# Optimization experiments

Measured on AMD Instinct MI355X. Metric: run time of the kernel, lower is better.

## Reference

```python
import jax, jax.numpy as jnp
import numpy as np

B, S, I, H = 64, 512, 512, 1024


def setup_inputs() -> dict:
    key = jax.random.key(0)
    ks = jax.random.split(key, 5)
    bound = 1.0 / np.sqrt(H)  # nn.GRUCell default init
    u = lambda k, shape: jax.random.uniform(k, shape, jnp.float32, -bound, bound)
    return {
        "input": jax.random.normal(ks[0], (B, S, I), jnp.float32),
        "state": jnp.zeros((B, H), jnp.float32),
        "weight_ih": u(ks[1], (3 * H, I)),
        "weight_hh": u(ks[2], (3 * H, H)),
        "bias_ih": u(ks[3], (3 * H,)),
        "bias_hh": u(ks[4], (3 * H,)),
        "gamma_ih": jnp.ones((3 * H,), jnp.float32),
        "gamma_hh": jnp.ones((3 * H,), jnp.float32),
    }


def _ln_x(x, g, b):
    # kefirski's _layer_norm_x: (x - mean) / std (unbiased std, eps=0)
    mean = jnp.mean(x, axis=-1, keepdims=True)
    std = jnp.std(x, axis=-1, keepdims=True, ddof=1)
    return g * ((x - mean) / std) + b


def _ln_h(x, g, b):
    # kefirski's _layer_norm_h: mean-subtraction only
    return g * (x - jnp.mean(x, axis=-1, keepdims=True)) + b


def reference(input, state, weight_ih, weight_hh, bias_ih, bias_hh, gamma_ih, gamma_hh):
    Hd = state.shape[-1]
    # Input-side projections + LN are h-independent -> precompute over all timesteps
    ih = jnp.einsum("bsi,gi->bsg", input, weight_ih)  # [B,S,3H]
    ih_rz = _ln_x(ih[..., : 2 * Hd], gamma_ih[: 2 * Hd], bias_ih[: 2 * Hd])  # [B,S,2H]
    ih_n = _ln_x(ih[..., 2 * Hd :], gamma_ih[2 * Hd :], bias_ih[2 * Hd :])  # [B,S,H]

    def step(h, xs):
        irz, inn = xs  # [B,2H], [B,H]
        hh = h @ weight_hh.T  # [B,3H]
        hh_rz = _ln_h(hh[:, : 2 * Hd], gamma_hh[: 2 * Hd], bias_hh[: 2 * Hd])
        hh_n = _ln_h(hh[:, 2 * Hd :], gamma_hh[2 * Hd :], bias_hh[2 * Hd :])
        rz = jax.nn.sigmoid(irz + hh_rz)
        r, z = rz[:, :Hd], rz[:, Hd:]
        n = jnp.tanh(inn + r * hh_n)
        h_new = (1.0 - z) * n + z * h
        return h_new, h_new

    final_state, outs = jax.lax.scan(
        step, state, (ih_rz.transpose(1, 0, 2), ih_n.transpose(1, 0, 2))
    )
    return outs.transpose(1, 0, 2), final_state  # [B,S,H], [B,H]
```

## Files before the change

kernel.cpp:

```cpp
#include <hip/hip_runtime.h>
#include <stdint.h>
#include <stddef.h>

#define B_  64
#define S_  512
#define I_  512
#define H_  1024
#define G_  3072
#define NWG 64
#define CPW 32

typedef short short8 __attribute__((ext_vector_type(8)));
typedef float f32x4  __attribute__((ext_vector_type(4)));
typedef unsigned short u16x4 __attribute__((ext_vector_type(4)));

__device__ __forceinline__ unsigned short f32_to_bf16(float f){
  unsigned u = __builtin_bit_cast(unsigned, f);
  u = (u + 0x7FFFu + ((u >> 16) & 1u)) >> 16;
  return (unsigned short)u;
}
__device__ __forceinline__ float bf16_to_f32(unsigned short s){
  unsigned u = ((unsigned)s) << 16;
  return __builtin_bit_cast(float, u);
}
__device__ __forceinline__ float sig_(float x){ return 1.0f/(1.0f + __expf(-x)); }
__device__ __forceinline__ float tanh_(float x){
  float ax = fabsf(x);
  float t = __expf(-2.0f*ax);
  float r = (1.0f - t)/(1.0f + t);
  return copysignf(r, x);
}

__device__ __forceinline__ short8 ldg16_coh(const unsigned short* p){
  short8 r;
  asm volatile("global_load_dwordx4 %0, %1, off sc0 sc1" : "=v"(r) : "v"(p) : "memory");
  return r;
}
__device__ __forceinline__ void stg8_coh(unsigned short* p, u16x4 v){
  asm volatile("global_store_dwordx2 %0, %1, off sc0 sc1" :: "v"(p), "v"(v) : "memory");
}
__device__ __forceinline__ void stg4_coh(unsigned* p, unsigned v){
  asm volatile("global_store_dword %0, %1, off sc0 sc1" :: "v"(p), "v"(v) : "memory");
}
__device__ __forceinline__ unsigned ldg4_coh_wait(const unsigned* p){
  unsigned r;
  asm volatile("global_load_dword %0, %1, off sc0 sc1\n\ts_waitcnt vmcnt(0)"
               : "=v"(r) : "v"(p) : "memory");
  return r;
}
__device__ __forceinline__ u16x4 ldg8(const unsigned short* p){
  u16x4 r;
  asm volatile("global_load_dwordx2 %0, %1, off" : "=v"(r) : "v"(p) : "memory");
  return r;
}

__global__ __launch_bounds__(256) void k_cvt4(const float* __restrict__ src,
                                              unsigned short* __restrict__ dst, int n4){
  int i = blockIdx.x*blockDim.x + threadIdx.x;
  int st = gridDim.x*blockDim.x;
  for (; i < n4; i += st){
    f32x4 v = *(const f32x4*)(src + (size_t)i*4);
    u16x4 o;
    o[0]=f32_to_bf16(v[0]); o[1]=f32_to_bf16(v[1]);
    o[2]=f32_to_bf16(v[2]); o[3]=f32_to_bf16(v[3]);
    *(u16x4*)(dst + (size_t)i*4) = o;
  }
}

__global__ __launch_bounds__(256) void k_cmean(const float* __restrict__ whh,
                                               unsigned short* __restrict__ CM){
  int k = blockIdx.x*256 + threadIdx.x;
  float s0 = 0.f, s1 = 0.f;
  for (int j = 0; j < 2048; ++j) s0 += whh[(size_t)j*H_ + k];
  for (int j = 2048; j < 3072; ++j) s1 += whh[(size_t)j*H_ + k];
  CM[k]      = f32_to_bf16(s0 * (1.0f/2048.0f));
  CM[H_ + k] = f32_to_bf16(s1 * (1.0f/1024.0f));
  for (int r = 2; r < 16; ++r) CM[(size_t)r*H_ + k] = 0;
}

__global__ __launch_bounds__(256, 2) void k_gemm_ih(
    const unsigned short* __restrict__ X,
    const unsigned short* __restrict__ W,
    unsigned short* __restrict__ IH)
{
  __shared__ __align__(16) short As[128*32];
  __shared__ __align__(16) short Bs[128*32];
  int bid = blockIdx.x;
  int mt = bid / 24, nt = bid % 24;
  int tid = threadIdx.x, lane = tid & 63, wid = tid >> 6;
  int vr = wid >> 1, vc = wid & 1;
  int r0s = tid >> 2, r1s = r0s + 64;
  int sc = (tid & 3) * 8;
  const unsigned short* xa0 = X + (size_t)(mt*128 + r0s)*512 + sc;
  const unsigned short* xa1 = X + (size_t)(mt*128 + r1s)*512 + sc;
  const unsigned short* wb0 = W + (size_t)(nt*128 + r0s)*512 + sc;
  const unsigned short* wb1 = W + (size_t)(nt*128 + r1s)*512 + sc;

  f32x4 acc[4][4];
  #pragma unroll
  for (int m=0;m<4;m++)
    #pragma unroll
    for (int n=0;n<4;n++) acc[m][n] = (f32x4){0.f,0.f,0.f,0.f};

  short8 ra0 = *(const short8*)xa0;
  short8 ra1 = *(const short8*)xa1;
  short8 rb0 = *(const short8*)wb0;
  short8 rb1 = *(const short8*)wb1;
  int ko = (lane >> 4) * 8;

  for (int kt = 0; kt < 16; ++kt){
    __syncthreads();
    *(short8*)&As[r0s*32 + sc] = ra0;
    *(short8*)&As[r1s*32 + sc] = ra1;
    *(short8*)&Bs[r0s*32 + sc] = rb0;
    *(short8*)&Bs[r1s*32 + sc] = rb1;
    __syncthreads();
    if (kt < 15){
      ra0 = *(const short8*)(xa0 + (kt+1)*32);
      ra1 = *(const short8*)(xa1 + (kt+1)*32);
      rb0 = *(const short8*)(wb0 + (kt+1)*32);
      rb1 = *(const short8*)(wb1 + (kt+1)*32);
    }
    short8 af[4], bfr[4];
    #pragma unroll
    for (int m=0;m<4;m++) af[m]  = *(const short8*)&As[(vr*64 + m*16 + (lane&15))*32 + ko];
    #pragma unroll
    for (int n=0;n<4;n++) bfr[n] = *(const short8*)&Bs[(vc*64 + n*16 + (lane&15))*32 + ko];
    #pragma unroll
    for (int m=0;m<4;m++)
      #pragma unroll
      for (int n=0;n<4;n++)
        acc[m][n] = __builtin_amdgcn_mfma_f32_16x16x32_bf16(af[m], bfr[n], acc[m][n], 0,0,0);
  }
  int row0 = mt*128 + vr*64, col0 = nt*128 + vc*64;
  int rl = (lane >> 4) * 4, cl = lane & 15;
  #pragma unroll
  for (int m=0;m<4;m++)
    #pragma unroll
    for (int n=0;n<4;n++)
      #pragma unroll
      for (int r=0;r<4;r++){
        int row = row0 + m*16 + rl + r;
        int rowT = ((row & 511) << 6) | (row >> 9);
        IH[(size_t)rowT*G_ + (col0 + n*16 + cl)] = f32_to_bf16(acc[m][n][r]);
      }
}

__global__ __launch_bounds__(256) void k_ln(
    unsigned short* __restrict__ IH,
    const float* __restrict__ gih,
    const float* __restrict__ bih)
{
  __shared__ float red[4][4];
  int row = blockIdx.x, tid = threadIdx.x, lane = tid & 63, wid = tid >> 6;
  unsigned short* p = IH + (size_t)row * G_;
  float xv[3][4];
  #pragma unroll
  for (int q=0;q<3;q++){
    u16x4 v = *(const u16x4*)(p + (tid + q*256)*4);
    #pragma unroll
    for (int j=0;j<4;j++) xv[q][j] = bf16_to_f32(v[j]);
  }
  float s0=0, q0=0, s1=0, q1=0;
  #pragma unroll
  for (int q=0;q<2;q++)
    #pragma unroll
    for (int j=0;j<4;j++){ s0 += xv[q][j]; q0 += xv[q][j]*xv[q][j]; }
  #pragma unroll
  for (int j=0;j<4;j++){ s1 += xv[2][j]; q1 += xv[2][j]*xv[2][j]; }
  #pragma unroll
  for (int off=32; off>0; off>>=1){
    s0 += __shfl_down(s0, off, 64);
    q0 += __shfl_down(q0, off, 64);
    s1 += __shfl_down(s1, off, 64);
    q1 += __shfl_down(q1, off, 64);
  }
  if (lane == 0){ red[wid][0]=s0; red[wid][1]=q0; red[wid][2]=s1; red[wid][3]=q1; }
  __syncthreads();
  float S0 = red[0][0]+red[1][0]+red[2][0]+red[3][0];
  float Q0 = red[0][1]+red[1][1]+red[2][1]+red[3][1];
  float S1 = red[0][2]+red[1][2]+red[2][2]+red[3][2];
  float Q1 = red[0][3]+red[1][3]+red[2][3]+red[3][3];
  float m0 = S0 * (1.0f/2048.0f);
  float rs0 = rsqrtf(fmaxf((Q0 - S0*m0) * (1.0f/2047.0f), 1e-20f));
  float m1 = S1 * (1.0f/1024.0f);
  float rs1 = rsqrtf(fmaxf((Q1 - S1*m1) * (1.0f/1023.0f), 1e-20f));
  #pragma unroll
  for (int q=0;q<3;q++){
    int base = (tid + q*256)*4;
    u16x4 o;
    #pragma unroll
    for (int j=0;j<4;j++){
      int col = base + j;
      float y = (q<2) ? (xv[q][j]-m0)*rs0 : (xv[q][j]-m1)*rs1;
      o[j] = f32_to_bf16(gih[col]*y + bih[col]);
    }
    *(u16x4*)(p + base) = o;
  }
}

__global__ __launch_bounds__(256, 1) void k_gru(
    const unsigned short* __restrict__ IH,
    const unsigned short* __restrict__ WHH,
    const unsigned short* __restrict__ CM,
    unsigned short* __restrict__ HB,
    const float* __restrict__ ghh,
    const float* __restrict__ bhh,
    const float* __restrict__ state,
    float* __restrict__ out,
    unsigned* __restrict__ FLAGS)
{
  __shared__ float PSUM[4][112][34];
  const int g = blockIdx.x & 31;
  const int p = blockIdx.x >> 5;
  const int tid = threadIdx.x;
  const int lane = tid & 63;
  const int wv = tid >> 6;
  const int l15 = lane & 15;
  const int lho = (lane >> 4) << 3;
  const int colbase = g * CPW;
  const int rowbase = p * 32;

  short8 bfr[7][8];
  #pragma unroll
  for (int ct = 0; ct < 7; ++ct){
    const unsigned short* src = (ct < 6)
        ? (WHH + (size_t)((ct>>1)*H_ + colbase + (ct&1)*16 + l15)*H_)
        : (CM + (size_t)l15*H_);
    #pragma unroll
    for (int ks = 0; ks < 8; ++ks)
      bfr[ct][ks] = *(const short8*)(src + wv*256 + ks*32 + lho);
  }

  const int b_ = tid & 31;
  const int cq = tid >> 5;
  const int c0 = colbase + cq*4;
  const int gb = rowbase + b_;
  float gr[4],gz[4],gn[4],br_[4],bz_[4],bn_[4],hv[4];
  #pragma unroll
  for (int j = 0; j < 4; ++j){
    gr[j] = ghh[c0+j];   gz[j] = ghh[H_+c0+j];   gn[j] = ghh[2*H_+c0+j];
    br_[j]= bhh[c0+j];   bz_[j]= bhh[H_+c0+j];   bn_[j]= bhh[2*H_+c0+j];
    hv[j] = state[(size_t)gb*H_ + c0 + j];
  }

  const unsigned* myflag = FLAGS + (p*32 + (lane & 31))*16;
  int cur = 0;

  for (int t = 0; t < S_; ++t){
    const unsigned short* ihp = IH + ((size_t)t*B_ + gb)*G_;
    u16x4 ir  = ldg8(ihp + c0);
    u16x4 izv = ldg8(ihp + H_ + c0);
    u16x4 inv = ldg8(ihp + 2*H_ + c0);

    for (;;){
      unsigned v = ldg4_coh_wait(myflag);
      if (__all((int)(v >= (unsigned)t))) break;
    }

    const unsigned short* hb = HB + cur*(B_*H_);
    short8 af[8][2];
    #pragma unroll
    for (int ks = 0; ks < 8; ++ks)
      #pragma unroll
      for (int rt = 0; rt < 2; ++rt)
        af[ks][rt] = ldg16_coh(hb + (size_t)(rowbase + rt*16 + l15)*H_ + wv*256 + ks*32 + lho);

    f32x4 acc[7][2];
    #pragma unroll
    for (int ct = 0; ct < 7; ++ct)
      #pragma unroll
      for (int rt = 0; rt < 2; ++rt)
        acc[ct][rt] = (f32x4){0.f,0.f,0.f,0.f};

    #pragma unroll
    for (int ks = 0; ks < 8; ++ks){
      asm volatile("s_waitcnt vmcnt(%0)" :: "i"(14 - 2*ks) : "memory");
      __builtin_amdgcn_sched_barrier(0);
      #pragma unroll
      for (int rt = 0; rt < 2; ++rt)
        #pragma unroll
        for (int ct = 0; ct < 7; ++ct)
          acc[ct][rt] = __builtin_amdgcn_mfma_f32_16x16x32_bf16(af[ks][rt], bfr[ct][ks], acc[ct][rt], 0,0,0);
    }

    #pragma unroll
    for (int ct = 0; ct < 7; ++ct)
      #pragma unroll
      for (int rt = 0; rt < 2; ++rt)
        *(f32x4*)&PSUM[wv][ct*16 + l15][rt*16 + (lane>>4)*4] = acc[ct][rt];
    __syncthreads();

    float hhr[4]={0,0,0,0}, hhz[4]={0,0,0,0}, hhn[4]={0,0,0,0};
    float mrz = 0.f, mn = 0.f;
    #pragma unroll
    for (int w = 0; w < 4; ++w){
      #pragma unroll
      for (int j = 0; j < 4; ++j){
        hhr[j] += PSUM[w][cq*4 + j][b_];
        hhz[j] += PSUM[w][32 + cq*4 + j][b_];
        hhn[j] += PSUM[w][64 + cq*4 + j][b_];
      }
      mrz += PSUM[w][96][b_];
      mn  += PSUM[w][97][b_];
    }
    f32x4 ho;
    #pragma unroll
    for (int j = 0; j < 4; ++j){
      float R = sig_(bf16_to_f32(ir[j])  + gr[j]*(hhr[j]-mrz) + br_[j]);
      float Z = sig_(bf16_to_f32(izv[j]) + gz[j]*(hhz[j]-mrz) + bz_[j]);
      float N = tanh_(bf16_to_f32(inv[j]) + R*(gn[j]*(hhn[j]-mn) + bn_[j]));
      hv[j] = (1.0f - Z)*N + Z*hv[j];
      ho[j] = hv[j];
    }
    u16x4 h16;
    #pragma unroll
    for (int j = 0; j < 4; ++j) h16[j] = f32_to_bf16(hv[j]);
    stg8_coh(HB + (cur^1)*(B_*H_) + (size_t)gb*H_ + c0, h16);

    asm volatile("s_waitcnt vmcnt(0)" ::: "memory");
    __syncthreads();
    if (tid == 0) stg4_coh((unsigned*)(FLAGS + (p*32 + g)*16), (unsigned)(t+1));
    *(f32x4*)(out + ((size_t)gb*S_ + t)*H_ + c0) = ho;
    cur ^= 1;
  }
  #pragma unroll
  for (int j = 0; j < 4; ++j)
    out[(size_t)B_*S_*H_ + (size_t)gb*H_ + c0 + j] = hv[j];
}

extern "C" void kernel_launch(void* const* d_in, const int* in_sizes, int n_in,
                              void* d_out, int out_size, void* d_ws, size_t ws_size,
                              hipStream_t stream){
  (void)in_sizes; (void)n_in; (void)out_size; (void)ws_size;
  const float* x   = (const float*)d_in[0];
  const float* st  = (const float*)d_in[1];
  const float* wih = (const float*)d_in[2];
  const float* whh = (const float*)d_in[3];
  const float* bih = (const float*)d_in[4];
  const float* bhh = (const float*)d_in[5];
  const float* gih = (const float*)d_in[6];
  const float* ghh = (const float*)d_in[7];
  float* out = (float*)d_out;
  char* ws = (char*)d_ws;

  unsigned short* IH    = (unsigned short*)(ws);
  unsigned short* X16   = (unsigned short*)(ws + 201326592ull);
  unsigned short* WIH16 = (unsigned short*)(ws + 234881024ull);
  unsigned short* WHH16 = (unsigned short*)(ws + 238026752ull);
  unsigned short* CM16  = (unsigned short*)(ws + 244318208ull);
  unsigned short* HB    = (unsigned short*)(ws + 244350976ull);
  unsigned*       FLAGS = (unsigned*)      (ws + 244613120ull);

  hipMemsetAsync(FLAGS, 0, 4096, stream);
  k_cvt4<<<2048, 256, 0, stream>>>(x,   X16,   4194304);
  k_cvt4<<<1024, 256, 0, stream>>>(wih, WIH16, 393216);
  k_cvt4<<<1024, 256, 0, stream>>>(whh, WHH16, 786432);
  k_cvt4<<<64,   256, 0, stream>>>(st,  HB,    16384);
  k_cmean<<<4,   256, 0, stream>>>(whh, CM16);
  k_gemm_ih<<<6144, 256, 0, stream>>>(X16, WIH16, IH);
  k_ln<<<32768, 256, 0, stream>>>(IH, gih, bih);
  k_gru<<<NWG, 256, 0, stream>>>(IH, WHH16, CM16, HB, ghh, bhh, st, out, FLAGS);
}
```

Measured before the change: 3.052 ms.

## Fuse input LayerNorm stats into GEMM epilogue and stream h loads per flag

Removes the separate LayerNorm kernel. The IH GEMM epilogue now accumulates per-row sum and sum-of-squares into a STAT buffer with atomics, and the recurrent kernel applies the normalization on the fly when it loads IH. The flag wait is also reworked: each lane polls a specific producer's flag and issues its h-state loads for a k-slice as soon as that producer is ready, instead of waiting for all producers first. This saves a full read/write pass over the large IH buffer and may overlap synchronization with loads. In exchange it adds float atomics, extra per-step normalization arithmetic, and stats computed from fp32 accumulators rather than the bf16-rounded values.

```diff
diff --git a/kernel.cpp b/kernel.cpp
--- a/kernel.cpp
+++ b/kernel.cpp
@@ -42,10 +42,9 @@
 __device__ __forceinline__ void stg4_coh(unsigned* p, unsigned v){
   asm volatile("global_store_dword %0, %1, off sc0 sc1" :: "v"(p), "v"(v) : "memory");
 }
-__device__ __forceinline__ unsigned ldg4_coh_wait(const unsigned* p){
+__device__ __forceinline__ unsigned ldg4_coh(const unsigned* p){
   unsigned r;
-  asm volatile("global_load_dword %0, %1, off sc0 sc1\n\ts_waitcnt vmcnt(0)"
-               : "=v"(r) : "v"(p) : "memory");
+  asm volatile("global_load_dword %0, %1, off sc0 sc1" : "=v"(r) : "v"(p) : "memory");
   return r;
 }
 __device__ __forceinline__ u16x4 ldg8(const unsigned short* p){
@@ -81,7 +80,8 @@
 __global__ __launch_bounds__(256, 2) void k_gemm_ih(
     const unsigned short* __restrict__ X,
     const unsigned short* __restrict__ W,
-    unsigned short* __restrict__ IH)
+    unsigned short* __restrict__ IH,
+    float* __restrict__ STAT)
 {
   __shared__ __align__(16) short As[128*32];
   __shared__ __align__(16) short Bs[128*32];
@@ -144,59 +144,27 @@
         int rowT = ((row & 511) << 6) | (row >> 9);
         IH[(size_t)rowT*G_ + (col0 + n*16 + cl)] = f32_to_bf16(acc[m][n][r]);
       }
-}
-
-__global__ __launch_bounds__(256) void k_ln(
-    unsigned short* __restrict__ IH,
-    const float* __restrict__ gih,
-    const float* __restrict__ bih)
-{
-  __shared__ float red[4][4];
-  int row = blockIdx.x, tid = threadIdx.x, lane = tid & 63, wid = tid >> 6;
-  unsigned short* p = IH + (size_t)row * G_;
-  float xv[3][4];
-  #pragma unroll
-  for (int q=0;q<3;q++){
-    u16x4 v = *(const u16x4*)(p + (tid + q*256)*4);
-    #pragma unroll
-    for (int j=0;j<4;j++) xv[q][j] = bf16_to_f32(v[j]);
-  }
-  float s0=0, q0=0, s1=0, q1=0;
-  #pragma unroll
-  for (int q=0;q<2;q++)
-    #pragma unroll
-    for (int j=0;j<4;j++){ s0 += xv[q][j]; q0 += xv[q][j]*xv[q][j]; }
-  #pragma unroll
-  for (int j=0;j<4;j++){ s1 += xv[2][j]; q1 += xv[2][j]*xv[2][j]; }
-  #pragma unroll
-  for (int off=32; off>0; off>>=1){
-    s0 += __shfl_down(s0, off, 64);
-    q0 += __shfl_down(q0, off, 64);
-    s1 += __shfl_down(s1, off, 64);
-    q1 += __shfl_down(q1, off, 64);
-  }
-  if (lane == 0){ red[wid][0]=s0; red[wid][1]=q0; red[wid][2]=s1; red[wid][3]=q1; }
-  __syncthreads();
-  float S0 = red[0][0]+red[1][0]+red[2][0]+red[3][0];
-  float Q0 = red[0][1]+red[1][1]+red[2][1]+red[3][1];
-  float S1 = red[0][2]+red[1][2]+red[2][2]+red[3][2];
-  float Q1 = red[0][3]+red[1][3]+red[2][3]+red[3][3];
-  float m0 = S0 * (1.0f/2048.0f);
-  float rs0 = rsqrtf(fmaxf((Q0 - S0*m0) * (1.0f/2047.0f), 1e-20f));
-  float m1 = S1 * (1.0f/1024.0f);
-  float rs1 = rsqrtf(fmaxf((Q1 - S1*m1) * (1.0f/1023.0f), 1e-20f));
-  #pragma unroll
-  for (int q=0;q<3;q++){
-    int base = (tid + q*256)*4;
-    u16x4 o;
-    #pragma unroll
-    for (int j=0;j<4;j++){
-      int col = base + j;
-      float y = (q<2) ? (xv[q][j]-m0)*rs0 : (xv[q][j]-m1)*rs1;
-      o[j] = f32_to_bf16(gih[col]*y + bih[col]);
+
+  const int soff = (nt < 16) ? 0 : 2;
+  #pragma unroll
+  for (int m=0;m<4;m++)
+    #pragma unroll
+    for (int r=0;r<4;r++){
+      float s1 = 0.f, s2 = 0.f;
+      #pragma unroll
+      for (int n=0;n<4;n++){ float v = acc[m][n][r]; s1 += v; s2 += v*v; }
+      #pragma unroll
+      for (int off=1; off<16; off<<=1){
+        s1 += __shfl_xor(s1, off, 16);
+        s2 += __shfl_xor(s2, off, 16);
+      }
+      if (cl == 0){
+        int row = row0 + m*16 + rl + r;
+        float* sp = STAT + (size_t)row*4 + soff;
+        atomicAdd(sp,     s1);
+        atomicAdd(sp + 1, s2);
+      }
     }
-    *(u16x4*)(p + base) = o;
-  }
 }
 
 __global__ __launch_bounds__(256, 1) void k_gru(
@@ -206,6 +174,9 @@
     unsigned short* __restrict__ HB,
     const float* __restrict__ ghh,
     const float* __restrict__ bhh,
+    const float* __restrict__ gih,
+    const float* __restrict__ bih,
+    const float* __restrict__ STAT,
     const float* __restrict__ state,
     float* __restrict__ out,
     unsigned* __restrict__ FLAGS)
@@ -236,35 +207,50 @@
   const int cq = tid >> 5;
   const int c0 = colbase + cq*4;
   const int gb = rowbase + b_;
-  float gr[4],gz[4],gn[4],br_[4],bz_[4],bn_[4],hv[4];
+  float gr[4],gz[4],gn[4],br_[4],bz_[4],bn_[4];
+  float gir[4],giz[4],gin[4],bir[4],biz[4],bin[4],hv[4];
   #pragma unroll
   for (int j = 0; j < 4; ++j){
-    gr[j] = ghh[c0+j];   gz[j] = ghh[H_+c0+j];   gn[j] = ghh[2*H_+c0+j];
-    br_[j]= bhh[c0+j];   bz_[j]= bhh[H_+c0+j];   bn_[j]= bhh[2*H_+c0+j];
-    hv[j] = state[(size_t)gb*H_ + c0 + j];
-  }
-
-  const unsigned* myflag = FLAGS + (p*32 + (lane & 31))*16;
-  int cur = 0;
+    int col = c0 + j;
+    gr[j] = ghh[col];   gz[j] = ghh[H_+col];   gn[j] = ghh[2*H_+col];
+    br_[j]= bhh[col];   bz_[j]= bhh[H_+col];   bn_[j]= bhh[2*H_+col];
+    gir[j]= gih[col];   giz[j]= gih[H_+col];   gin[j]= gih[2*H_+col];
+    bir[j]= bih[col];   biz[j]= bih[H_+col];   bin[j]= bih[2*H_+col];
+    hv[j] = state[(size_t)gb*H_ + col];
+  }
+
+  const unsigned* fbase = FLAGS + (size_t)(p*32 + wv*8 + (lane & 7))*16;
+  unsigned* pubflag = FLAGS + (size_t)(p*32 + g)*16;
 
   for (int t = 0; t < S_; ++t){
+    const unsigned short* hbR = HB + (t & 1)*(B_*H_);
+    unsigned short*       hbW = (unsigned short*)HB + ((t+1) & 1)*(B_*H_);
+
     const unsigned short* ihp = IH + ((size_t)t*B_ + gb)*G_;
     u16x4 ir  = ldg8(ihp + c0);
     u16x4 izv = ldg8(ihp + H_ + c0);
     u16x4 inv = ldg8(ihp + 2*H_ + c0);
-
-    for (;;){
-      unsigned v = ldg4_coh_wait(myflag);
-      if (__all((int)(v >= (unsigned)t))) break;
-    }
-
-    const unsigned short* hb = HB + cur*(B_*H_);
+    f32x4 sv = *(const f32x4*)(STAT + (((size_t)gb << 9) | t)*4);
+
     short8 af[8][2];
-    #pragma unroll
-    for (int ks = 0; ks < 8; ++ks)
-      #pragma unroll
-      for (int rt = 0; rt < 2; ++rt)
-        af[ks][rt] = ldg16_coh(hb + (size_t)(rowbase + rt*16 + l15)*H_ + wv*256 + ks*32 + lho);
+    unsigned pend = 0xFFu;
+    do {
+      unsigned v = ldg4_coh(fbase);
+      asm volatile("s_waitcnt vmcnt(0)" ::: "memory");
+      __builtin_amdgcn_sched_barrier(0);
+      unsigned long long bl = __ballot((int)(v >= (unsigned)t));
+      unsigned newly = ((unsigned)bl & 0xFFu) & pend;
+      #pragma unroll
+      for (int ks = 0; ks < 8; ++ks){
+        if (newly & (1u << ks)){
+          af[ks][0] = ldg16_coh(hbR + (size_t)(rowbase + l15)*H_      + wv*256 + ks*32 + lho);
+          af[ks][1] = ldg16_coh(hbR + (size_t)(rowbase + 16 + l15)*H_ + wv*256 + ks*32 + lho);
+        }
+      }
+      pend &= ~newly;
+    } while (pend);
+    asm volatile("s_waitcnt vmcnt(0)" ::: "memory");
+    __builtin_amdgcn_sched_barrier(0);
 
     f32x4 acc[7][2];
     #pragma unroll
@@ -272,17 +258,13 @@
       #pragma unroll
       for (int rt = 0; rt < 2; ++rt)
         acc[ct][rt] = (f32x4){0.f,0.f,0.f,0.f};
-
-    #pragma unroll
-    for (int ks = 0; ks < 8; ++ks){
-      asm volatile("s_waitcnt vmcnt(%0)" :: "i"(14 - 2*ks) : "memory");
-      __builtin_amdgcn_sched_barrier(0);
+    #pragma unroll
+    for (int ks = 0; ks < 8; ++ks)
       #pragma unroll
       for (int rt = 0; rt < 2; ++rt)
         #pragma unroll
         for (int ct = 0; ct < 7; ++ct)
           acc[ct][rt] = __builtin_amdgcn_mfma_f32_16x16x32_bf16(af[ks][rt], bfr[ct][ks], acc[ct][rt], 0,0,0);
-    }
 
     #pragma unroll
     for (int ct = 0; ct < 7; ++ct)
@@ -304,25 +286,30 @@
       mrz += PSUM[w][96][b_];
       mn  += PSUM[w][97][b_];
     }
+    float m0 = sv[0] * (1.0f/2048.0f);
+    float rs0 = rsqrtf(fmaxf((sv[1] - sv[0]*m0) * (1.0f/2047.0f), 1e-20f));
+    float m1 = sv[2] * (1.0f/1024.0f);
+    float rs1 = rsqrtf(fmaxf((sv[3] - sv[2]*m1) * (1.0f/1023.0f), 1e-20f));
     f32x4 ho;
+    u16x4 h16;
     #pragma unroll
     for (int j = 0; j < 4; ++j){
-      float R = sig_(bf16_to_f32(ir[j])  + gr[j]*(hhr[j]-mrz) + br_[j]);
-      float Z = sig_(bf16_to_f32(izv[j]) + gz[j]*(hhz[j]-mrz) + bz_[j]);
-      float N = tanh_(bf16_to_f32(inv[j]) + R*(gn[j]*(hhn[j]-mn) + bn_[j]));
+      float xr = gir[j]*(bf16_to_f32(ir[j])  - m0)*rs0 + bir[j];
+      float xz = giz[j]*(bf16_to_f32(izv[j]) - m0)*rs0 + biz[j];
+      float xn = gin[j]*(bf16_to_f32(inv[j]) - m1)*rs1 + bin[j];
+      float R = sig_(xr + gr[j]*(hhr[j]-mrz) + br_[j]);
+      float Z = sig_(xz + gz[j]*(hhz[j]-mrz) + bz_[j]);
+      float N = tanh_(xn + R*(gn[j]*(hhn[j]-mn) + bn_[j]));
       hv[j] = (1.0f - Z)*N + Z*hv[j];
       ho[j] = hv[j];
+      h16[j] = f32_to_bf16(hv[j]);
     }
-    u16x4 h16;
-    #pragma unroll
-    for (int j = 0; j < 4; ++j) h16[j] = f32_to_bf16(hv[j]);
-    stg8_coh(HB + (cur^1)*(B_*H_) + (size_t)gb*H_ + c0, h16);
+    *(f32x4*)(out + ((size_t)gb*S_ + t)*H_ + c0) = ho;
+    stg8_coh(hbW + (size_t)gb*H_ + c0, h16);
 
     asm volatile("s_waitcnt vmcnt(0)" ::: "memory");
     __syncthreads();
-    if (tid == 0) stg4_coh((unsigned*)(FLAGS + (p*32 + g)*16), (unsigned)(t+1));
-    *(f32x4*)(out + ((size_t)gb*S_ + t)*H_ + c0) = ho;
-    cur ^= 1;
+    if (tid == 0) stg4_coh(pubflag, (unsigned)(t+1));
   }
   #pragma unroll
   for (int j = 0; j < 4; ++j)
@@ -351,14 +338,15 @@
   unsigned short* CM16  = (unsigned short*)(ws + 244318208ull);
   unsigned short* HB    = (unsigned short*)(ws + 244350976ull);
   unsigned*       FLAGS = (unsigned*)      (ws + 244613120ull);
+  float*          STAT  = (float*)         (ws + 244617216ull);
 
   hipMemsetAsync(FLAGS, 0, 4096, stream);
+  hipMemsetAsync(STAT, 0, 524288, stream);
   k_cvt4<<<2048, 256, 0, stream>>>(x,   X16,   4194304);
   k_cvt4<<<1024, 256, 0, stream>>>(wih, WIH16, 393216);
   k_cvt4<<<1024, 256, 0, stream>>>(whh, WHH16, 786432);
   k_cvt4<<<64,   256, 0, stream>>>(st,  HB,    16384);
   k_cmean<<<4,   256, 0, stream>>>(whh, CM16);
-  k_gemm_ih<<<6144, 256, 0, stream>>>(X16, WIH16, IH);
-  k_ln<<<32768, 256, 0, stream>>>(IH, gih, bih);
-  k_gru<<<NWG, 256, 0, stream>>>(IH, WHH16, CM16, HB, ghh, bhh, st, out, FLAGS);
-}
+  k_gemm_ih<<<6144, 256, 0, stream>>>(X16, WIH16, IH, STAT);
+  k_gru<<<NWG, 256, 0, stream>>>(IH, WHH16, CM16, HB, ghh, bhh, gih, bih, STAT, st, out, FLAGS);
+}
```

New measurement: 3.710 ms. 1.22x slower.
